# Kernel optimization log

Hardware: AMD Instinct MI355X
Metric: run time of the kernel (lower is better)

## Reference

```python
import jax, jax.numpy as jnp
import numpy as np

B, C, H, W = 8, 8, 640, 640
M = 16  # max instance ids per image (0 = background)
EPS = 1e-12


def setup_inputs() -> dict:
    key = jax.random.key(0)
    k1, k2, k3, k4, k5 = jax.random.split(key, 5)
    outputs = jax.random.normal(k1, (B, C, H, W), dtype=jnp.float32)
    gt_texts = jax.random.randint(k2, (B, H, W), 0, M)
    gt_kernels = jax.random.randint(k3, (B, H, W), 0, M)
    gt_tops = jax.random.randint(k4, (B, H, W), 0, M)
    gt_bots = jax.random.randint(k5, (B, H, W), 0, M)
    return dict(outputs=outputs, gt_texts=gt_texts, gt_kernels=gt_kernels,
                gt_tops=gt_tops, gt_bots=gt_bots)


def _pull_push(outputs, gt_texts, gt_kernels):
    b = outputs.shape[0]
    n = outputs.shape[2] * outputs.shape[3]
    # similarity embedding per pixel: [B, N, 4]
    sim = outputs[:, 4:].reshape(b, 4, n).transpose(0, 2, 1)
    kt = gt_kernels.reshape(b, n)
    tt = gt_texts.reshape(b, n)
    off = jnp.arange(b, dtype=kt.dtype)[:, None] * M
    ids_k = (kt + off).reshape(-1)
    ids_t = (tt + off).reshape(-1)
    sim_flat = sim.reshape(b * n, 4)
    ones = jnp.ones((b * n,), sim.dtype)

    # per-instance kernel centroids G (segment mean over kernel pixels)
    sum_k = jax.ops.segment_sum(sim_flat, ids_k, num_segments=b * M).reshape(b, M, 4)
    cnt_k = jax.ops.segment_sum(ones, ids_k, num_segments=b * M).reshape(b, M)
    G = sum_k / jnp.maximum(cnt_k, 1.0)[..., None]  # [B, M, 4]
    # instance valid iff it has kernel pixels and idx >= 1 (0 is background)
    valid = (cnt_k > 0) & (jnp.arange(M)[None, :] >= 1)

    # pull loss: per text pixel, distance to its instance's kernel centroid
    G_pix = jnp.take_along_axis(G, tt[..., None], axis=1)  # [B, N, 4]
    d = jnp.sqrt(((sim - G_pix) ** 2).sum(-1) + EPS) - 0.5  # [B, N]
    l_pix = jnp.log1p(jnp.maximum(d, 0.0) ** 2).reshape(-1)
    sum_t = jax.ops.segment_sum(l_pix, ids_t, num_segments=b * M).reshape(b, M)
    cnt_t = jax.ops.segment_sum(ones, ids_t, num_segments=b * M).reshape(b, M)
    per_inst = sum_t / jnp.maximum(cnt_t, 1.0)  # mean over each instance's text pixels
    nv = valid.sum(-1).astype(sim.dtype)
    loss_pull = (per_inst * valid).sum(-1) / jnp.maximum(nv, 1.0)

    # push loss: pairwise centroid separation, pairs (i < j) of valid instances
    diff = G[:, :, None, :] - G[:, None, :, :]  # [B, M, M, 4]
    dk = jnp.sqrt((diff ** 2).sum(-1) + EPS)
    val = jnp.log1p(jnp.maximum(3.0 - dk, 0.0) ** 2)
    iu = jnp.triu(jnp.ones((M, M), bool), 1)
    pm = valid[:, :, None] & valid[:, None, :] & iu[None]
    push_sum = (val * pm).sum((1, 2))
    denom = nv * (nv - 1.0)  # matches original normalization n*(n-1)
    loss_push = jnp.where(nv > 1, push_sum / jnp.maximum(denom, 1.0), 0.0)
    return loss_pull, loss_push


def reference(outputs, gt_texts, gt_kernels, gt_tops, gt_bots):
    # gt_tops/gt_bots are consumed by broken (non-contributing) branches in the
    # original code; the returned losses depend only on gt_texts/gt_kernels.
    return _pull_push(outputs, gt_texts, gt_kernels)
```

## Files before the change

kernel.cpp:

```cpp
#include <hip/hip_runtime.h>
#include <math.h>

#define BB 8
#define MI 16
#define NN 409600
#define CEPS 1e-12f
#define GPB 200
#define TPB 256

#define WS_PS   0
#define WS_G    (BB*GPB*80)
#define WS_VAL  (WS_G + BB*MI*4)
#define WS_PP   (WS_VAL + BB*MI)

__global__ __launch_bounds__(TPB, 6) void k_sums(
    const float* __restrict__ outputs, const int* __restrict__ gt_kernels,
    float* __restrict__ ws) {
  __shared__ float red[4][64][17];
  __shared__ float cbuf[MI];
  const int b = blockIdx.y, blk = blockIdx.x, tid = threadIdx.x;
  const int wv = tid >> 6, lane = tid & 63;
  const int mb = wv * 4;

  float acc[16];
#pragma unroll
  for (int i = 0; i < 16; i++) acc[i] = 0.f;
  unsigned int cnt[4] = {0u, 0u, 0u, 0u};

  const float* s0 = outputs + (size_t)(b * 8 + 4) * NN;
  const int* gkb = gt_kernels + (size_t)b * NN;

#pragma unroll 2
  for (int it = 0; it < 8; it++) {
    const int pix = blk * 2048 + it * 256 + lane * 4;
    const int4 id4 = *(const int4*)(gkb + pix);
    const float4 x0 = *(const float4*)(s0 + pix);
    const float4 x1 = *(const float4*)(s0 + NN + pix);
    const float4 x2 = *(const float4*)(s0 + 2 * NN + pix);
    const float4 x3 = *(const float4*)(s0 + 3 * NN + pix);
#define SLOTK(IDC, XC)                                                       \
    {                                                                        \
      const int id = id4.IDC - mb;                                           \
      _Pragma("unroll")                                                      \
      for (int j = 0; j < 4; j++) {                                          \
        const bool e = (id == j);                                            \
        cnt[j] += (unsigned)__popcll(__ballot(e));          \
        const float f = e ? 1.f : 0.f;                                       \
        acc[0 * 4 + j] += f * x0.XC;                                         \
        acc[1 * 4 + j] += f * x1.XC;                                         \
        acc[2 * 4 + j] += f * x2.XC;                                         \
        acc[3 * 4 + j] += f * x3.XC;                                         \
      }                                                                      \
    }
    SLOTK(x, x) SLOTK(y, y) SLOTK(z, z) SLOTK(w, w)
#undef SLOTK
  }

#pragma unroll
  for (int v = 0; v < 16; v++) red[wv][lane][v] = acc[v];
  if (lane == 0) {
#pragma unroll
    for (int j = 0; j < 4; j++) cbuf[mb + j] = (float)cnt[j];
  }
  __syncthreads();
  if (tid < 80) {
    const int m = tid / 5, c = tid % 5;
    const int w = m >> 2, j = m & 3;
    float s;
    if (c < 4) {
      const int vi = c * 4 + j;
      s = 0.f;
#pragma unroll 8
      for (int l = 0; l < 64; l++) s += red[w][(l + tid) & 63][vi];
    } else {
      s = cbuf[m];
    }
    ws[WS_PS + (size_t)(b * GPB + blk) * 80 + tid] = s;
  }
}

__global__ void k_finG(float* __restrict__ ws) {
  __shared__ float part[5][80];
  __shared__ float tot[80];
  const int b = blockIdx.x, t = threadIdx.x;
  const int v = t % 80, h = t / 80;
  float s = 0.f;
  const float* src = ws + WS_PS + (size_t)(b * GPB + h * 40) * 80 + v;
#pragma unroll
  for (int k = 0; k < 40; k++) s += src[(size_t)k * 80];
  part[h][v] = s;
  __syncthreads();
  if (t < 80) tot[t] = part[0][t] + part[1][t] + part[2][t] + part[3][t] + part[4][t];
  __syncthreads();
  if (t < MI) {
    const float cnt = tot[t * 5 + 4];
    const float inv = 1.f / fmaxf(cnt, 1.f);
    float4 g;
    g.x = tot[t * 5 + 0] * inv;
    g.y = tot[t * 5 + 1] * inv;
    g.z = tot[t * 5 + 2] * inv;
    g.w = tot[t * 5 + 3] * inv;
    ((float4*)(ws + WS_G))[b * MI + t] = g;
    ws[WS_VAL + b * MI + t] = (cnt > 0.f && t >= 1) ? 1.f : 0.f;
  }
}

__global__ __launch_bounds__(TPB, 6) void k_pull(
    const float* __restrict__ outputs, const int* __restrict__ gt_texts,
    float* __restrict__ ws) {
  __shared__ float4 sG[MI];
  __shared__ float red[4][64][17];
  __shared__ float cbuf[4][MI];
  const int b = blockIdx.y, blk = blockIdx.x, tid = threadIdx.x;
  const int wv = tid >> 6, lane = tid & 63;
  if (tid < MI) sG[tid] = ((const float4*)(ws + WS_G))[b * MI + tid];
  __syncthreads();

  float al[16];
#pragma unroll
  for (int m = 0; m < MI; m++) al[m] = 0.f;
  unsigned int cw[16];
#pragma unroll
  for (int m = 0; m < MI; m++) cw[m] = 0u;

  const float* s0 = outputs + (size_t)(b * 8 + 4) * NN;
  const int* ttb = gt_texts + (size_t)b * NN;

#pragma unroll
  for (int it = 0; it < 2; it++) {
    const int pix = blk * 2048 + it * 1024 + tid * 4;
    const int4 id4 = *(const int4*)(ttb + pix);
    const float4 x0 = *(const float4*)(s0 + pix);
    const float4 x1 = *(const float4*)(s0 + NN + pix);
    const float4 x2 = *(const float4*)(s0 + 2 * NN + pix);
    const float4 x3 = *(const float4*)(s0 + 3 * NN + pix);
#define SLOTP(IDC, XC)                                                       \
    {                                                                        \
      const int id = id4.IDC;                                                \
      const float4 g = sG[id];                                               \
      const float d0 = x0.XC - g.x, d1 = x1.XC - g.y;                        \
      const float d2 = x2.XC - g.z, d3 = x3.XC - g.w;                        \
      const float dist = sqrtf(d0*d0 + d1*d1 + d2*d2 + d3*d3 + CEPS) - 0.5f; \
      const float dm = fmaxf(dist, 0.f);                                     \
      const float l = __logf(1.f + dm * dm);                                 \
      _Pragma("unroll")                                                      \
      for (int m = 0; m < MI; m++) {                                         \
        const bool e = (id == m);                                            \
        cw[m] += (unsigned)__popcll(__ballot(e));           \
        al[m] += e ? l : 0.f;                                                \
      }                                                                      \
    }
    SLOTP(x, x) SLOTP(y, y) SLOTP(z, z) SLOTP(w, w)
#undef SLOTP
  }

#pragma unroll
  for (int v = 0; v < 16; v++) red[wv][lane][v] = al[v];
  if (lane == 0) {
#pragma unroll
    for (int m = 0; m < MI; m++) cbuf[wv][m] = (float)cw[m];
  }
  __syncthreads();
  if (tid < 32) {
    const int m = tid >> 1, c = tid & 1;
    float s = 0.f;
    if (c == 0) {
#pragma unroll
      for (int w = 0; w < 4; w++)
#pragma unroll 8
        for (int l = 0; l < 64; l++) s += red[w][(l + tid) & 63][m];
    } else {
      s = cbuf[0][m] + cbuf[1][m] + cbuf[2][m] + cbuf[3][m];
    }
    ws[WS_PP + (size_t)(b * GPB + blk) * 32 + tid] = s;
  }
}

__global__ void k_final(const float* __restrict__ ws, float* __restrict__ out) {
  __shared__ float part[8][32];
  __shared__ float tot[32];
  const int b = blockIdx.x, t = threadIdx.x;
  const int v = t & 31, h = t >> 5;
  float s = 0.f;
  const float* src = ws + WS_PP + (size_t)(b * GPB + h * 25) * 32 + v;
#pragma unroll
  for (int k = 0; k < 25; k++) s += src[(size_t)k * 32];
  part[h][v] = s;
  __syncthreads();
  if (t < 32) {
    float x = 0.f;
#pragma unroll
    for (int hh = 0; hh < 8; hh++) x += part[hh][t];
    tot[t] = x;
  }
  __syncthreads();
  if (t == 0) {
    const float* G = ws + WS_G;
    const float* valid = ws + WS_VAL;
    float nv = 0.f;
    for (int m = 0; m < MI; m++) nv += valid[b * MI + m];
    float pull = 0.f;
    for (int m = 0; m < MI; m++) {
      const float per = tot[m * 2] / fmaxf(tot[m * 2 + 1], 1.f);
      pull += per * valid[b * MI + m];
    }
    pull /= fmaxf(nv, 1.f);
    float push = 0.f;
    for (int i = 0; i < MI; i++) {
      if (valid[b * MI + i] == 0.f) continue;
      for (int j = i + 1; j < MI; j++) {
        if (valid[b * MI + j] == 0.f) continue;
        float d2 = CEPS;
        for (int c = 0; c < 4; c++) {
          const float df = G[(b * MI + i) * 4 + c] - G[(b * MI + j) * 4 + c];
          d2 += df * df;
        }
        const float dk = sqrtf(d2);
        const float tt = fmaxf(3.f - dk, 0.f);
        push += log1pf(tt * tt);
      }
    }
    const float denom = nv * (nv - 1.f);
    push = (nv > 1.f) ? push / fmaxf(denom, 1.f) : 0.f;
    out[b] = pull;
    out[BB + b] = push;
  }
}

extern "C" void kernel_launch(void* const* d_in, const int* in_sizes, int n_in,
                              void* d_out, int out_size, void* d_ws, size_t ws_size,
                              hipStream_t stream) {
  const float* outputs = (const float*)d_in[0];
  const int* gt_texts = (const int*)d_in[1];
  const int* gt_kernels = (const int*)d_in[2];
  float* ws = (float*)d_ws;
  float* out = (float*)d_out;

  dim3 grid(GPB, BB);
  k_sums<<<grid, TPB, 0, stream>>>(outputs, gt_kernels, ws);
  k_finG<<<BB, 400, 0, stream>>>(ws);
  k_pull<<<grid, TPB, 0, stream>>>(outputs, gt_texts, ws);
  k_final<<<BB, 256, 0, stream>>>(ws, out);
}
```

Baseline: 248.6 us.

## Fold centroid finalize into pull/final kernels and split pixels across waves in k_sums

Removes the separate centroid-finalize kernel; each pull block and the final kernel now redundantly reduce the per-block partial sums from the workspace to rebuild centroids. k_sums assigns each wave its own pixel quarter with accumulators for all 16 ids, instead of every wave rereading all pixels for 4 ids, which cuts redundant global loads. In exchange, register pressure rises, there are more shared-memory reduction rounds, and each pull block adds a serial workspace reduction before it starts its main work.

Result: slower. 301.2 us (+21.2%).

```diff
diff --git a/kernel.cpp b/kernel.cpp
--- a/kernel.cpp
+++ b/kernel.cpp
@@ -9,30 +9,31 @@
 #define TPB 256
 
 #define WS_PS   0
-#define WS_G    (BB*GPB*80)
-#define WS_VAL  (WS_G + BB*MI*4)
-#define WS_PP   (WS_VAL + BB*MI)
-
-__global__ __launch_bounds__(TPB, 6) void k_sums(
+#define WS_PP   (BB*GPB*80)
+
+__global__ __launch_bounds__(TPB, 4) void k_sums(
     const float* __restrict__ outputs, const int* __restrict__ gt_kernels,
     float* __restrict__ ws) {
   __shared__ float red[4][64][17];
-  __shared__ float cbuf[MI];
+  __shared__ float part2[4][16];
+  __shared__ float cbuf[4][MI];
+  __shared__ float obuf[80];
   const int b = blockIdx.y, blk = blockIdx.x, tid = threadIdx.x;
   const int wv = tid >> 6, lane = tid & 63;
-  const int mb = wv * 4;
-
-  float acc[16];
-#pragma unroll
-  for (int i = 0; i < 16; i++) acc[i] = 0.f;
-  unsigned int cnt[4] = {0u, 0u, 0u, 0u};
+
+  float acc[64];
+#pragma unroll
+  for (int i = 0; i < 64; i++) acc[i] = 0.f;
+  unsigned int cnt[16];
+#pragma unroll
+  for (int m = 0; m < MI; m++) cnt[m] = 0u;
 
   const float* s0 = outputs + (size_t)(b * 8 + 4) * NN;
   const int* gkb = gt_kernels + (size_t)b * NN;
 
-#pragma unroll 2
-  for (int it = 0; it < 8; it++) {
-    const int pix = blk * 2048 + it * 256 + lane * 4;
+#pragma unroll
+  for (int it = 0; it < 2; it++) {
+    const int pix = blk * 2048 + wv * 512 + it * 256 + lane * 4;
     const int4 id4 = *(const int4*)(gkb + pix);
     const float4 x0 = *(const float4*)(s0 + pix);
     const float4 x1 = *(const float4*)(s0 + NN + pix);
@@ -40,69 +41,54 @@
     const float4 x3 = *(const float4*)(s0 + 3 * NN + pix);
 #define SLOTK(IDC, XC)                                                       \
     {                                                                        \
-      const int id = id4.IDC - mb;                                           \
+      const int id = id4.IDC;                                                \
       _Pragma("unroll")                                                      \
-      for (int j = 0; j < 4; j++) {                                          \
-        const bool e = (id == j);                                            \
-        cnt[j] += (unsigned)__popcll(__ballot(e));          \
+      for (int m = 0; m < MI; m++) {                                         \
+        const bool e = (id == m);                                            \
+        cnt[m] += (unsigned)__popcll(__ballot(e));          \
         const float f = e ? 1.f : 0.f;                                       \
-        acc[0 * 4 + j] += f * x0.XC;                                         \
-        acc[1 * 4 + j] += f * x1.XC;                                         \
-        acc[2 * 4 + j] += f * x2.XC;                                         \
-        acc[3 * 4 + j] += f * x3.XC;                                         \
+        acc[m * 4 + 0] += f * x0.XC;                                         \
+        acc[m * 4 + 1] += f * x1.XC;                                         \
+        acc[m * 4 + 2] += f * x2.XC;                                         \
+        acc[m * 4 + 3] += f * x3.XC;                                         \
       }                                                                      \
     }
     SLOTK(x, x) SLOTK(y, y) SLOTK(z, z) SLOTK(w, w)
 #undef SLOTK
   }
 
-#pragma unroll
-  for (int v = 0; v < 16; v++) red[wv][lane][v] = acc[v];
   if (lane == 0) {
 #pragma unroll
-    for (int j = 0; j < 4; j++) cbuf[mb + j] = (float)cnt[j];
-  }
-  __syncthreads();
-  if (tid < 80) {
-    const int m = tid / 5, c = tid % 5;
-    const int w = m >> 2, j = m & 3;
-    float s;
-    if (c < 4) {
-      const int vi = c * 4 + j;
-      s = 0.f;
-#pragma unroll 8
-      for (int l = 0; l < 64; l++) s += red[w][(l + tid) & 63][vi];
-    } else {
-      s = cbuf[m];
-    }
-    ws[WS_PS + (size_t)(b * GPB + blk) * 80 + tid] = s;
-  }
-}
-
-__global__ void k_finG(float* __restrict__ ws) {
-  __shared__ float part[5][80];
-  __shared__ float tot[80];
-  const int b = blockIdx.x, t = threadIdx.x;
-  const int v = t % 80, h = t / 80;
-  float s = 0.f;
-  const float* src = ws + WS_PS + (size_t)(b * GPB + h * 40) * 80 + v;
-#pragma unroll
-  for (int k = 0; k < 40; k++) s += src[(size_t)k * 80];
-  part[h][v] = s;
-  __syncthreads();
-  if (t < 80) tot[t] = part[0][t] + part[1][t] + part[2][t] + part[3][t] + part[4][t];
-  __syncthreads();
-  if (t < MI) {
-    const float cnt = tot[t * 5 + 4];
-    const float inv = 1.f / fmaxf(cnt, 1.f);
-    float4 g;
-    g.x = tot[t * 5 + 0] * inv;
-    g.y = tot[t * 5 + 1] * inv;
-    g.z = tot[t * 5 + 2] * inv;
-    g.w = tot[t * 5 + 3] * inv;
-    ((float4*)(ws + WS_G))[b * MI + t] = g;
-    ws[WS_VAL + b * MI + t] = (cnt > 0.f && t >= 1) ? 1.f : 0.f;
-  }
+    for (int m = 0; m < MI; m++) cbuf[wv][m] = (float)cnt[m];
+  }
+
+#pragma unroll
+  for (int r = 0; r < 4; r++) {
+#pragma unroll
+    for (int k = 0; k < 16; k++) red[wv][lane][k] = acc[r * 16 + k];
+    __syncthreads();
+    if (tid < 64) {
+      const int k = tid & 15, q = tid >> 4;
+      float s = 0.f;
+#pragma unroll
+      for (int l = 0; l < 16; l++) {
+        const int ln = q * 16 + l;
+        s += red[0][ln][k] + red[1][ln][k] + red[2][ln][k] + red[3][ln][k];
+      }
+      part2[q][k] = s;
+    }
+    __syncthreads();
+    if (tid < 16) {
+      const int m = 4 * r + (tid >> 2), c = tid & 3;
+      obuf[m * 5 + c] = part2[0][tid] + part2[1][tid] + part2[2][tid] + part2[3][tid];
+    }
+    __syncthreads();
+  }
+  if (tid < 16)
+    obuf[tid * 5 + 4] = cbuf[0][tid] + cbuf[1][tid] + cbuf[2][tid] + cbuf[3][tid];
+  __syncthreads();
+  if (tid < 80)
+    ws[WS_PS + (size_t)(b * GPB + blk) * 80 + tid] = obuf[tid];
 }
 
 __global__ __launch_bounds__(TPB, 6) void k_pull(
@@ -111,10 +97,35 @@
   __shared__ float4 sG[MI];
   __shared__ float red[4][64][17];
   __shared__ float cbuf[4][MI];
+  __shared__ float gpart[3][80];
+  __shared__ float tot80[80];
   const int b = blockIdx.y, blk = blockIdx.x, tid = threadIdx.x;
   const int wv = tid >> 6, lane = tid & 63;
-  if (tid < MI) sG[tid] = ((const float4*)(ws + WS_G))[b * MI + tid];
-  __syncthreads();
+
+  {
+    const int v = tid % 80, h = tid / 80;
+    if (h < 3) {
+      const int nb = (h < 2) ? 67 : 66;
+      const float* src = ws + WS_PS + (size_t)(b * GPB + h * 67) * 80 + v;
+      float s = 0.f;
+      for (int k = 0; k < nb; k++) s += src[(size_t)k * 80];
+      gpart[h][v] = s;
+    }
+    __syncthreads();
+    if (tid < 80) tot80[tid] = gpart[0][tid] + gpart[1][tid] + gpart[2][tid];
+    __syncthreads();
+    if (tid < MI) {
+      const float cntk = tot80[tid * 5 + 4];
+      const float inv = 1.f / fmaxf(cntk, 1.f);
+      float4 g;
+      g.x = tot80[tid * 5 + 0] * inv;
+      g.y = tot80[tid * 5 + 1] * inv;
+      g.z = tot80[tid * 5 + 2] * inv;
+      g.w = tot80[tid * 5 + 3] * inv;
+      sG[tid] = g;
+    }
+    __syncthreads();
+  }
 
   float al[16];
 #pragma unroll
@@ -177,9 +188,38 @@
 }
 
 __global__ void k_final(const float* __restrict__ ws, float* __restrict__ out) {
+  __shared__ float gpart[3][80];
+  __shared__ float tot80[80];
   __shared__ float part[8][32];
   __shared__ float tot[32];
+  __shared__ float sG[MI * 4];
+  __shared__ float svalid[MI];
   const int b = blockIdx.x, t = threadIdx.x;
+
+  {
+    const int v = t % 80, h = t / 80;
+    if (h < 3) {
+      const int nb = (h < 2) ? 67 : 66;
+      const float* src = ws + WS_PS + (size_t)(b * GPB + h * 67) * 80 + v;
+      float s = 0.f;
+      for (int k = 0; k < nb; k++) s += src[(size_t)k * 80];
+      gpart[h][v] = s;
+    }
+    __syncthreads();
+    if (t < 80) tot80[t] = gpart[0][t] + gpart[1][t] + gpart[2][t];
+    __syncthreads();
+    if (t < MI) {
+      const float cntk = tot80[t * 5 + 4];
+      const float inv = 1.f / fmaxf(cntk, 1.f);
+      sG[t * 4 + 0] = tot80[t * 5 + 0] * inv;
+      sG[t * 4 + 1] = tot80[t * 5 + 1] * inv;
+      sG[t * 4 + 2] = tot80[t * 5 + 2] * inv;
+      sG[t * 4 + 3] = tot80[t * 5 + 3] * inv;
+      svalid[t] = (cntk > 0.f && t >= 1) ? 1.f : 0.f;
+    }
+    __syncthreads();
+  }
+
   const int v = t & 31, h = t >> 5;
   float s = 0.f;
   const float* src = ws + WS_PP + (size_t)(b * GPB + h * 25) * 32 + v;
@@ -195,24 +235,22 @@
   }
   __syncthreads();
   if (t == 0) {
-    const float* G = ws + WS_G;
-    const float* valid = ws + WS_VAL;
     float nv = 0.f;
-    for (int m = 0; m < MI; m++) nv += valid[b * MI + m];
+    for (int m = 0; m < MI; m++) nv += svalid[m];
     float pull = 0.f;
     for (int m = 0; m < MI; m++) {
       const float per = tot[m * 2] / fmaxf(tot[m * 2 + 1], 1.f);
-      pull += per * valid[b * MI + m];
+      pull += per * svalid[m];
     }
     pull /= fmaxf(nv, 1.f);
     float push = 0.f;
     for (int i = 0; i < MI; i++) {
-      if (valid[b * MI + i] == 0.f) continue;
+      if (svalid[i] == 0.f) continue;
       for (int j = i + 1; j < MI; j++) {
-        if (valid[b * MI + j] == 0.f) continue;
+        if (svalid[j] == 0.f) continue;
         float d2 = CEPS;
         for (int c = 0; c < 4; c++) {
-          const float df = G[(b * MI + i) * 4 + c] - G[(b * MI + j) * 4 + c];
+          const float df = sG[i * 4 + c] - sG[j * 4 + c];
           d2 += df * df;
         }
         const float dk = sqrtf(d2);
@@ -238,7 +276,6 @@
 
   dim3 grid(GPB, BB);
   k_sums<<<grid, TPB, 0, stream>>>(outputs, gt_kernels, ws);
-  k_finG<<<BB, 400, 0, stream>>>(ws);
   k_pull<<<grid, TPB, 0, stream>>>(outputs, gt_texts, ws);
   k_final<<<BB, 256, 0, stream>>>(ws, out);
 }
```

## Partition kernel-sum pixels across waves instead of instance ids

Applied to the files above, without the earlier changes.

In k_sums, each wave now handles its own quarter of the block's pixels and accumulates all 16 instance ids, with 64 float and 16 count accumulators per thread. Previously each wave read every pixel and kept only 4 ids. The change removes the 4x redundant global/cache loads of embeddings and labels across the waves of a block. In exchange it raises register pressure (occupancy hint lowered from 6 to 4) and replaces the single LDS reduction with four reduction rounds, each needing extra barriers.

Measured after the change: 253.0 us. Within noise of the previous version (+1.8%).

```diff
diff --git a/kernel.cpp b/kernel.cpp
--- a/kernel.cpp
+++ b/kernel.cpp
@@ -13,26 +13,29 @@
 #define WS_VAL  (WS_G + BB*MI*4)
 #define WS_PP   (WS_VAL + BB*MI)
 
-__global__ __launch_bounds__(TPB, 6) void k_sums(
+__global__ __launch_bounds__(TPB, 4) void k_sums(
     const float* __restrict__ outputs, const int* __restrict__ gt_kernels,
     float* __restrict__ ws) {
   __shared__ float red[4][64][17];
-  __shared__ float cbuf[MI];
+  __shared__ float part2[4][16];
+  __shared__ float cbuf[4][MI];
+  __shared__ float obuf[80];
   const int b = blockIdx.y, blk = blockIdx.x, tid = threadIdx.x;
   const int wv = tid >> 6, lane = tid & 63;
-  const int mb = wv * 4;
-
-  float acc[16];
-#pragma unroll
-  for (int i = 0; i < 16; i++) acc[i] = 0.f;
-  unsigned int cnt[4] = {0u, 0u, 0u, 0u};
+
+  float acc[64];
+#pragma unroll
+  for (int i = 0; i < 64; i++) acc[i] = 0.f;
+  unsigned int cnt[16];
+#pragma unroll
+  for (int m = 0; m < MI; m++) cnt[m] = 0u;
 
   const float* s0 = outputs + (size_t)(b * 8 + 4) * NN;
   const int* gkb = gt_kernels + (size_t)b * NN;
 
-#pragma unroll 2
-  for (int it = 0; it < 8; it++) {
-    const int pix = blk * 2048 + it * 256 + lane * 4;
+#pragma unroll
+  for (int it = 0; it < 2; it++) {
+    const int pix = blk * 2048 + wv * 512 + it * 256 + lane * 4;
     const int4 id4 = *(const int4*)(gkb + pix);
     const float4 x0 = *(const float4*)(s0 + pix);
     const float4 x1 = *(const float4*)(s0 + NN + pix);
@@ -40,43 +43,54 @@
     const float4 x3 = *(const float4*)(s0 + 3 * NN + pix);
 #define SLOTK(IDC, XC)                                                       \
     {                                                                        \
-      const int id = id4.IDC - mb;                                           \
+      const int id = id4.IDC;                                                \
       _Pragma("unroll")                                                      \
-      for (int j = 0; j < 4; j++) {                                          \
-        const bool e = (id == j);                                            \
-        cnt[j] += (unsigned)__popcll(__ballot(e));          \
+      for (int m = 0; m < MI; m++) {                                         \
+        const bool e = (id == m);                                            \
+        cnt[m] += (unsigned)__popcll(__ballot(e));          \
         const float f = e ? 1.f : 0.f;                                       \
-        acc[0 * 4 + j] += f * x0.XC;                                         \
-        acc[1 * 4 + j] += f * x1.XC;                                         \
-        acc[2 * 4 + j] += f * x2.XC;                                         \
-        acc[3 * 4 + j] += f * x3.XC;                                         \
+        acc[m * 4 + 0] += f * x0.XC;                                         \
+        acc[m * 4 + 1] += f * x1.XC;                                         \
+        acc[m * 4 + 2] += f * x2.XC;                                         \
+        acc[m * 4 + 3] += f * x3.XC;                                         \
       }                                                                      \
     }
     SLOTK(x, x) SLOTK(y, y) SLOTK(z, z) SLOTK(w, w)
 #undef SLOTK
   }
 
-#pragma unroll
-  for (int v = 0; v < 16; v++) red[wv][lane][v] = acc[v];
   if (lane == 0) {
 #pragma unroll
-    for (int j = 0; j < 4; j++) cbuf[mb + j] = (float)cnt[j];
-  }
-  __syncthreads();
-  if (tid < 80) {
-    const int m = tid / 5, c = tid % 5;
-    const int w = m >> 2, j = m & 3;
-    float s;
-    if (c < 4) {
-      const int vi = c * 4 + j;
-      s = 0.f;
-#pragma unroll 8
-      for (int l = 0; l < 64; l++) s += red[w][(l + tid) & 63][vi];
-    } else {
-      s = cbuf[m];
-    }
-    ws[WS_PS + (size_t)(b * GPB + blk) * 80 + tid] = s;
-  }
+    for (int m = 0; m < MI; m++) cbuf[wv][m] = (float)cnt[m];
+  }
+
+#pragma unroll
+  for (int r = 0; r < 4; r++) {
+#pragma unroll
+    for (int k = 0; k < 16; k++) red[wv][lane][k] = acc[r * 16 + k];
+    __syncthreads();
+    if (tid < 64) {
+      const int k = tid & 15, q = tid >> 4;
+      float s = 0.f;
+#pragma unroll
+      for (int l = 0; l < 16; l++) {
+        const int ln = q * 16 + l;
+        s += red[0][ln][k] + red[1][ln][k] + red[2][ln][k] + red[3][ln][k];
+      }
+      part2[q][k] = s;
+    }
+    __syncthreads();
+    if (tid < 16) {
+      const int m = 4 * r + (tid >> 2), c = tid & 3;
+      obuf[m * 5 + c] = part2[0][tid] + part2[1][tid] + part2[2][tid] + part2[3][tid];
+    }
+    __syncthreads();
+  }
+  if (tid < 16)
+    obuf[tid * 5 + 4] = cbuf[0][tid] + cbuf[1][tid] + cbuf[2][tid] + cbuf[3][tid];
+  __syncthreads();
+  if (tid < 80)
+    ws[WS_PS + (size_t)(b * GPB + blk) * 80 + tid] = obuf[tid];
 }
 
 __global__ void k_finG(float* __restrict__ ws) {
```
